# Kernel tuning notes

Measured on AMD Instinct MI355X. Metric: run time of the kernel, lower is better.

Reference implementation:

```python
import jax, jax.numpy as jnp
import numpy as np

# Semantic hierarchy configuration (stand-in for semantic_softmax_processor)
GROUP_SIZES = [8192, 4096, 2048, 1024, 512, 256, 128, 64, 32, 16]
NORM_FACTORS = [0.1] * len(GROUP_SIZES)
TOPK_CAP = 500
TEMPERATURE = 1.0
TOTAL_CLASSES = sum(GROUP_SIZES)  # 16368
BATCH = 1024


def setup_inputs() -> dict:
    key = jax.random.key(0)
    k1, k2, k3 = jax.random.split(key, 3)
    logits = jax.random.normal(k1, (BATCH, TOTAL_CLASSES), dtype=jnp.float32)
    logits_teacher = jax.random.normal(k2, (BATCH, TOTAL_CLASSES), dtype=jnp.float32)
    targets = jax.random.randint(k3, (BATCH,), 0, TOTAL_CLASSES, dtype=jnp.int64)
    return {"logits": logits, "logits_teacher": logits_teacher, "targets": targets}


def _group_kd_loss(s_logits, t_logits, temperature):
    # s_logits, t_logits: [B, C_i] for one semantic group
    B, C = t_logits.shape
    k = min(C, TOPK_CAP)
    # teacher top-k classes (sorted, largest)
    t_top, t_idx = jax.lax.top_k(t_logits, k)                 # [B, k]
    s_top = jnp.take_along_axis(s_logits, t_idx, axis=1)      # [B, k]
    log_p = jax.nn.log_softmax(s_top / temperature, axis=1)   # student log-probs
    log_q = jax.nn.log_softmax(t_top / temperature, axis=1)   # teacher log-probs
    q = jnp.exp(log_q)
    # KL(q || p), reduction='batchmean'
    kl = jnp.sum(q * (log_q - log_p)) / B
    return kl * temperature * temperature


def reference(logits, logits_teacher, targets):
    # targets are converted to semantic targets in the original module but are
    # never used in the loss computation (dead code) -> no effect on output.
    del targets
    total = jnp.float32(0.0)
    offset = 0
    for gsize, norm in zip(GROUP_SIZES, NORM_FACTORS):
        s_i = jax.lax.slice_in_dim(logits, offset, offset + gsize, axis=1)
        t_i = jax.lax.slice_in_dim(logits_teacher, offset, offset + gsize, axis=1)
        total = total + _group_kd_loss(s_i, t_i, TEMPERATURE) * norm
        offset += gsize
    return total
```

## Files before the change

### kernel.cpp

```cpp
#include <hip/hip_runtime.h>
#include <stdint.h>
#include <float.h>

#define TOTAL 16368
#define KSEL 500
#define Q0CAP 384
#define Q1CAP 704
#define G2CAP 768
#define NBUCKET 64

#define A_KV 0
#define A_SV 6144
#define A_IX 12288
#define B_KV 0
#define B_SV 5632
#define B_IX 11264
#define B_G2V 14080
#define B_G2I 17152
#define SMEM_BYTES 18688

__device__ __forceinline__ uint32_t fkey(float f) {
    uint32_t u = __float_as_uint(f);
    return (u & 0x80000000u) ? ~u : (u | 0x80000000u);
}
__device__ __forceinline__ float keyf(uint32_t k) {
    uint32_t u = (k & 0x80000000u) ? (k & 0x7FFFFFFFu) : ~k;
    return __uint_as_float(u);
}
__device__ __forceinline__ int lanerank(uint64_t m) {
    return __builtin_amdgcn_mbcnt_hi((uint32_t)(m >> 32),
           __builtin_amdgcn_mbcnt_lo((uint32_t)m, 0));
}
__device__ __forceinline__ int wave_sumi(int v) {
    #pragma unroll
    for (int o = 32; o > 0; o >>= 1) v += __shfl_xor(v, o, 64);
    return v;
}
__device__ __forceinline__ float wave_sumf(float v) {
    #pragma unroll
    for (int o = 32; o > 0; o >>= 1) v += __shfl_xor(v, o, 64);
    return v;
}
__device__ __forceinline__ float wave_maxf(float v) {
    #pragma unroll
    for (int o = 32; o > 0; o >>= 1) v = fmaxf(v, __shfl_xor(v, o, 64));
    return v;
}
__device__ __forceinline__ void lse_merge(float& m, float& l, float m2, float l2) {
    float M = fmaxf(m, m2);
    l = l * __expf(m - M) + l2 * __expf(m2 - M);
    m = M;
}

__device__ __noinline__ float wave_slow_kl(const float* __restrict__ t,
                                           const float* __restrict__ s, int C) {
    const int lane = threadIdx.x & 63;
    uint64_t lo = 0ull, hi = (1ull << 45), tau = 0ull;
    int cl = C, ch = 0;
    #pragma unroll 1
    for (int it = 0; it < 100; ++it) {
        uint64_t span = hi - lo;
        if (span <= 1ull) { tau = lo; break; }
        uint64_t mid;
        if (it & 1) mid = lo + (span >> 1);
        else {
            uint64_t st = span * (uint64_t)(cl - KSEL) / (uint64_t)(cl - ch);
            if (st < 1) st = 1;
            if (st > span - 1) st = span - 1;
            mid = lo + st;
        }
        int c = 0;
        #pragma unroll 1
        for (int i = lane; i < C; i += 64) {
            uint64_t ck = ((uint64_t)fkey(t[i]) << 13) | (uint64_t)(8191 - i);
            c += (ck > mid);
        }
        c = wave_sumi(c);
        if (c == KSEL) { tau = mid; break; }
        if (c > KSEL) { lo = mid; cl = c; } else { hi = mid; ch = c; }
    }
    float tmx = -FLT_MAX;
    for (int i = lane; i < C; i += 64) tmx = fmaxf(tmx, t[i]);
    tmx = wave_maxf(tmx);
    float St = 0.f, Stt = 0.f, Sts = 0.f, sm = -FLT_MAX;
    #pragma unroll 1
    for (int i = lane; i < C; i += 64) {
        float x = t[i];
        uint64_t ck = ((uint64_t)fkey(x) << 13) | (uint64_t)(8191 - i);
        if (ck > tau) {
            float e = __expf(x - tmx), v = s[i];
            St += e; Stt += e * x; Sts += e * v;
            sm = fmaxf(sm, v);
        }
    }
    St = wave_sumf(St); Stt = wave_sumf(Stt); Sts = wave_sumf(Sts); sm = wave_maxf(sm);
    float Ss = 0.f;
    #pragma unroll 1
    for (int i = lane; i < C; i += 64) {
        uint64_t ck = ((uint64_t)fkey(t[i]) << 13) | (uint64_t)(8191 - i);
        if (ck > tau) Ss += __expf(s[i] - sm);
    }
    Ss = wave_sumf(Ss);
    if (lane == 0)
        return (Stt - Sts) / St - tmx - __logf(St) + sm + __logf(Ss);
    return 0.f;
}

template <int CAP>
__device__ int slice_compact(const float* __restrict__ tq,
                             const float* __restrict__ sg,
                             float thr, int idx_off,
                             uint32_t* kv, float* sv, uint16_t* ix) {
    const int lane = threadIdx.x & 63;
    const float4* t4 = (const float4*)tq;
    float4 tb[8];
    #pragma unroll
    for (int u = 0; u < 8; ++u) tb[u] = t4[u * 64 + lane];
    int cnt = 0;
    #pragma unroll
    for (int u = 0; u < 8; ++u) {
        float tx[4] = {tb[u].x, tb[u].y, tb[u].z, tb[u].w};
        #pragma unroll
        for (int q = 0; q < 4; ++q) {
            bool p = tx[q] > thr;
            uint64_t m = __ballot(p);
            if (p) {
                int ofs = cnt + lanerank(m);
                if (ofs < CAP) {
                    kv[ofs] = fkey(tx[q]);
                    ix[ofs] = (uint16_t)((((u * 64 + lane) << 2) + q) + idx_off);
                }
            }
            cnt += (int)__popcll(m);
        }
    }
    if (cnt <= CAP) {
        for (int p = cnt + lane; p < CAP; p += 64) kv[p] = 0u;
        constexpr int NR = CAP / 64;
        float r[NR];
        #pragma unroll
        for (int j = 0; j < NR; ++j) {
            int p = lane + j * 64;
            r[j] = (p < cnt) ? sg[(int)ix[p]] : 0.f;
        }
        #pragma unroll
        for (int j = 0; j < NR; ++j) {
            int p = lane + j * 64;
            if (p < cnt) sv[p] = r[j];
        }
    }
    return cnt;
}

template <int S, int SEGCAP, int NS>
__device__ float seg_select(const uint32_t* __restrict__ kv,
                            const float* __restrict__ sv,
                            const uint16_t* __restrict__ ix,
                            const int* __restrict__ cnts, int C,
                            const float* __restrict__ tg,
                            const float* __restrict__ sg) {
    const int lane = threadIdx.x & 63;
    int tot = 0; bool bad = false;
    #pragma unroll
    for (int q = 0; q < S; ++q) {
        int c = cnts[q];
        tot += c;
        bad = bad || (c > SEGCAP);
    }
    if (bad || tot < KSEL) return wave_slow_kl(tg, sg, C);

    uint32_t key[NS];
    #pragma unroll
    for (int j = 0; j < NS; ++j) key[j] = kv[lane + j * 64];

    uint32_t kmx = 0u, kmn = 0xFFFFFFFFu;
    #pragma unroll
    for (int j = 0; j < NS; ++j) {
        uint32_t k = key[j];
        kmx = k > kmx ? k : kmx;
        if (k) kmn = k < kmn ? k : kmn;
    }
    #pragma unroll
    for (int o = 32; o > 0; o >>= 1) {
        uint32_t a = __shfl_xor(kmx, o, 64); kmx = a > kmx ? a : kmx;
        uint32_t b = __shfl_xor(kmn, o, 64); kmn = b < kmn ? b : kmn;
    }
    const float tmax = keyf(kmx);

    uint32_t lo = kmn - 1u, hi = kmx, tauhi = kmx;
    int cl = tot, ch = 0, cut = -1;
    bool exact = false;
    #pragma unroll 1
    for (int it = 0; it < 80; ++it) {
        uint32_t span = hi - lo;
        if (span <= 1u) break;
        uint32_t mid;
        if (!(it & 1)) {
            uint64_t st = (uint64_t)span * (uint32_t)(cl - KSEL) / (uint32_t)(cl - ch);
            if (st < 1) st = 1;
            if (st > span - 1) st = span - 1;
            mid = lo + (uint32_t)st;
        } else mid = lo + (span >> 1);
        int c = 0;
        #pragma unroll
        for (int j = 0; j < NS; ++j)
            c += (int)__popcll(__ballot(key[j] > mid));
        if (c == KSEL) { tauhi = mid; exact = true; break; }
        if (c > KSEL) { lo = mid; cl = c; } else { hi = mid; ch = c; }
    }
    if (!exact) {
        tauhi = hi;
        const int nT = KSEL - ch, nTie = cl - ch;
        if (nT >= nTie) cut = 0x7FFFFFFF;
        else {
            int l = -1, h = C - 1;
            #pragma unroll 1
            while (h - l > 1) {
                int m = (l + h) >> 1;
                int c = 0;
                #pragma unroll
                for (int j = 0; j < NS; ++j)
                    c += (int)__popcll(__ballot(key[j] == tauhi &&
                                                (int)ix[lane + j * 64] <= m));
                if (c >= nT) h = m; else l = m;
            }
            cut = h;
        }
    }

    uint32_t selm = 0u;
    if (cut == -1) {
        #pragma unroll
        for (int j = 0; j < NS; ++j) selm |= (key[j] > tauhi ? 1u : 0u) << j;
    } else if (cut == 0x7FFFFFFF) {
        #pragma unroll
        for (int j = 0; j < NS; ++j) selm |= (key[j] >= tauhi ? 1u : 0u) << j;
    } else {
        #pragma unroll
        for (int j = 0; j < NS; ++j) {
            bool sj = (key[j] > tauhi) ||
                      (key[j] == tauhi && (int)ix[lane + j * 64] <= cut);
            selm |= (sj ? 1u : 0u) << j;
        }
    }

    float St = 0.f, Stt = 0.f, Sts = 0.f, sm = -FLT_MAX;
    #pragma unroll
    for (int j = 0; j < NS; ++j) {
        if (selm & (1u << j)) {
            float tv = keyf(key[j]);
            float e = __expf(tv - tmax);
            float s = sv[lane + j * 64];
            St += e; Stt += e * tv; Sts += e * s;
            sm = fmaxf(sm, s);
        }
    }
    #pragma unroll
    for (int o = 32; o > 0; o >>= 1) {
        St  += __shfl_xor(St,  o, 64);
        Stt += __shfl_xor(Stt, o, 64);
        Sts += __shfl_xor(Sts, o, 64);
        sm = fmaxf(sm, __shfl_xor(sm, o, 64));
    }
    float Ss = 0.f;
    #pragma unroll
    for (int j = 0; j < NS; ++j)
        if (selm & (1u << j)) Ss += __expf(sv[lane + j * 64] - sm);
    Ss = wave_sumf(Ss);
    if (lane == 0)
        return (Stt - Sts) / St - tmax - __logf(St) + sm + __logf(Ss);
    return 0.f;
}

template <int NF4, int CAPT, int NST>
__device__ float big_wave(const float* __restrict__ tg, const float* __restrict__ s,
                          float thr, float* vals, uint16_t* idxs) {
    const int lane = threadIdx.x & 63;
    const float4* t4 = (const float4*)tg;
    constexpr int NB = NF4 / 8;
    int cnt = 0;
    float4 buf[8], nxt[8];
    #pragma unroll
    for (int u = 0; u < 8; ++u) buf[u] = t4[u * 64 + lane];
    #pragma unroll 1
    for (int b = 0; b < NB; ++b) {
        if (b + 1 < NB) {
            #pragma unroll
            for (int u = 0; u < 8; ++u)
                nxt[u] = t4[((b + 1) * 8 + u) * 64 + lane];
        }
        #pragma unroll
        for (int u = 0; u < 8; ++u) {
            float xs[4] = {buf[u].x, buf[u].y, buf[u].z, buf[u].w};
            #pragma unroll
            for (int q = 0; q < 4; ++q) {
                bool p = xs[q] > thr;
                uint64_t m = __ballot(p);
                if (p) {
                    int ofs = cnt + lanerank(m);
                    if (ofs < CAPT) {
                        vals[ofs] = xs[q];
                        idxs[ofs] = (uint16_t)((((b * 8 + u) * 64 + lane) << 2) + q);
                    }
                }
                cnt += (int)__popcll(m);
            }
        }
        if (b + 1 < NB) {
            #pragma unroll
            for (int u = 0; u < 8; ++u) buf[u] = nxt[u];
        }
    }
    if (cnt < KSEL || cnt > CAPT) return wave_slow_kl(tg, s, NF4 * 256);

    uint32_t key[NST];
    #pragma unroll
    for (int j = 0; j < NST; ++j) {
        int p = lane + j * 64;
        key[j] = (p < cnt) ? fkey(vals[p]) : 0u;
    }
    uint32_t kmx = 0u, kmn = 0xFFFFFFFFu;
    #pragma unroll
    for (int j = 0; j < NST; ++j) {
        uint32_t k = key[j];
        kmx = k > kmx ? k : kmx;
        if (k) kmn = k < kmn ? k : kmn;
    }
    #pragma unroll
    for (int o = 32; o > 0; o >>= 1) {
        uint32_t a = __shfl_xor(kmx, o, 64); kmx = a > kmx ? a : kmx;
        uint32_t b2 = __shfl_xor(kmn, o, 64); kmn = b2 < kmn ? b2 : kmn;
    }
    const float tmax = keyf(kmx);

    uint32_t lo = kmn - 1u, hi = kmx, tauhi = kmx;
    int cl = cnt, ch = 0, cut = -1;
    bool exact = false;
    #pragma unroll 1
    for (int it = 0; it < 80; ++it) {
        uint32_t span = hi - lo;
        if (span <= 1u) break;
        uint32_t mid;
        if (!(it & 1)) {
            uint64_t st = (uint64_t)span * (uint32_t)(cl - KSEL) / (uint32_t)(cl - ch);
            if (st < 1) st = 1;
            if (st > span - 1) st = span - 1;
            mid = lo + (uint32_t)st;
        } else mid = lo + (span >> 1);
        int c = 0;
        #pragma unroll
        for (int j = 0; j < NST; ++j)
            c += (int)__popcll(__ballot(key[j] > mid));
        if (c == KSEL) { tauhi = mid; exact = true; break; }
        if (c > KSEL) { lo = mid; cl = c; } else { hi = mid; ch = c; }
    }
    if (!exact) {
        tauhi = hi;
        const int nT = KSEL - ch, nTie = cl - ch;
        if (nT >= nTie) cut = 0x7FFFFFFF;
        else {
            int idxr[NST];
            #pragma unroll
            for (int j = 0; j < NST; ++j) {
                int p = lane + j * 64;
                idxr[j] = (p < cnt) ? (int)idxs[p] : 0x7FFF;
            }
            int l = -1, h = 8191;
            #pragma unroll 1
            while (h - l > 1) {
                int m = (l + h) >> 1;
                int c = 0;
                #pragma unroll
                for (int j = 0; j < NST; ++j)
                    c += (int)__popcll(__ballot(key[j] == tauhi && idxr[j] <= m));
                if (c >= nT) h = m; else l = m;
            }
            cut = h;
        }
    }

    uint32_t selm = 0u;
    if (cut == -1) {
        #pragma unroll
        for (int j = 0; j < NST; ++j) selm |= (key[j] > tauhi ? 1u : 0u) << j;
    } else if (cut == 0x7FFFFFFF) {
        #pragma unroll
        for (int j = 0; j < NST; ++j) selm |= (key[j] >= tauhi ? 1u : 0u) << j;
    } else {
        #pragma unroll
        for (int j = 0; j < NST; ++j) {
            int p = lane + j * 64;
            bool sj = (key[j] > tauhi) ||
                      (key[j] == tauhi && p < cnt && (int)idxs[p] <= cut);
            selm |= (sj ? 1u : 0u) << j;
        }
    }

    float svc[NST];
    #pragma unroll
    for (int j = 0; j < NST; ++j)
        svc[j] = (selm & (1u << j)) ? s[(int)idxs[lane + j * 64]] : 0.f;

    float St = 0.f, Stt = 0.f, Sts = 0.f, sm = -FLT_MAX;
    #pragma unroll
    for (int j = 0; j < NST; ++j) {
        if (selm & (1u << j)) {
            float tv = keyf(key[j]);
            float e = __expf(tv - tmax);
            St += e; Stt += e * tv; Sts += e * svc[j];
            sm = fmaxf(sm, svc[j]);
        }
    }
    #pragma unroll
    for (int o = 32; o > 0; o >>= 1) {
        St  += __shfl_xor(St,  o, 64);
        Stt += __shfl_xor(Stt, o, 64);
        Sts += __shfl_xor(Sts, o, 64);
        sm = fmaxf(sm, __shfl_xor(sm, o, 64));
    }
    float Ss = 0.f;
    #pragma unroll
    for (int j = 0; j < NST; ++j)
        if (selm & (1u << j)) Ss += __expf(svc[j] - sm);
    Ss = wave_sumf(Ss);
    if (lane == 0)
        return (Stt - Sts) / St - tmax - __logf(St) + sm + __logf(Ss);
    return 0.f;
}

template <int NS, class IdxF>
__device__ float select_accum(uint32_t (&key)[NS], IdxF idxOf, const float* svp) {
    const int lane = threadIdx.x & 63;
    uint32_t kmx = 0u, kmn = 0xFFFFFFFFu;
    #pragma unroll
    for (int j = 0; j < NS; ++j) {
        uint32_t k = key[j];
        kmx = k > kmx ? k : kmx;
        kmn = k < kmn ? k : kmn;
    }
    #pragma unroll
    for (int o = 32; o > 0; o >>= 1) {
        uint32_t a = __shfl_xor(kmx, o, 64); kmx = a > kmx ? a : kmx;
        uint32_t b = __shfl_xor(kmn, o, 64); kmn = b < kmn ? b : kmn;
    }
    const float tmax = keyf(kmx);

    uint32_t lo = kmn - 1u, hi = kmx, tauhi = kmx;
    int cl = NS * 64, ch = 0, cut = -1;
    bool exact = false;
    #pragma unroll 1
    for (int it = 0; it < 80; ++it) {
        uint32_t span = hi - lo;
        if (span <= 1u) break;
        uint32_t mid;
        if (!(it & 1)) {
            uint64_t st = (uint64_t)span * (uint32_t)(cl - KSEL) / (uint32_t)(cl - ch);
            if (st < 1) st = 1;
            if (st > span - 1) st = span - 1;
            mid = lo + (uint32_t)st;
        } else mid = lo + (span >> 1);
        int c = 0;
        #pragma unroll
        for (int j = 0; j < NS; ++j)
            c += (int)__popcll(__ballot(key[j] > mid));
        if (c == KSEL) { tauhi = mid; exact = true; break; }
        if (c > KSEL) { lo = mid; cl = c; } else { hi = mid; ch = c; }
    }
    if (!exact) {
        tauhi = hi;
        const int nT = KSEL - ch, nTie = cl - ch;
        if (nT >= nTie) cut = 0x7FFFFFFF;
        else {
            int l = -1, h = NS * 64 - 1;
            #pragma unroll 1
            while (h - l > 1) {
                int m = (l + h) >> 1;
                int c = 0;
                #pragma unroll
                for (int j = 0; j < NS; ++j)
                    c += (int)__popcll(__ballot(key[j] == tauhi && idxOf(j) <= m));
                if (c >= nT) h = m; else l = m;
            }
            cut = h;
        }
    }

    float St = 0.f, Stt = 0.f, Sts = 0.f, sm = -FLT_MAX;
    #pragma unroll
    for (int j = 0; j < NS; ++j) {
        uint32_t kj = key[j];
        bool sj = (kj > tauhi) || (kj == tauhi && idxOf(j) <= cut);
        if (sj) {
            float tv = keyf(kj);
            float e = __expf(tv - tmax);
            St += e; Stt += e * tv; Sts += e * svp[j];
            sm = fmaxf(sm, svp[j]);
        }
    }
    #pragma unroll
    for (int o = 32; o > 0; o >>= 1) {
        St  += __shfl_xor(St,  o, 64);
        Stt += __shfl_xor(Stt, o, 64);
        Sts += __shfl_xor(Sts, o, 64);
        sm = fmaxf(sm, __shfl_xor(sm, o, 64));
    }
    float Ss = 0.f;
    #pragma unroll
    for (int j = 0; j < NS; ++j) {
        uint32_t kj = key[j];
        bool sj = (kj > tauhi) || (kj == tauhi && idxOf(j) <= cut);
        if (sj) Ss += __expf(svp[j] - sm);
    }
    Ss = wave_sumf(Ss);
    if (lane == 0)
        return (Stt - Sts) / St - tmax - __logf(St) + sm + __logf(Ss);
    return 0.f;
}

template <int NJ>
__device__ float mid_wave(const float* __restrict__ t, const float* __restrict__ s) {
    const int lane = threadIdx.x & 63;
    const float4* t4 = (const float4*)t;
    const float4* s4 = (const float4*)s;
    uint32_t key[NJ];
    float svp[NJ];
    #pragma unroll
    for (int c = 0; c < NJ / 4; ++c) {
        float4 x = t4[lane + c * 64];
        float4 y = s4[lane + c * 64];
        key[4 * c + 0] = fkey(x.x); key[4 * c + 1] = fkey(x.y);
        key[4 * c + 2] = fkey(x.z); key[4 * c + 3] = fkey(x.w);
        svp[4 * c + 0] = y.x; svp[4 * c + 1] = y.y;
        svp[4 * c + 2] = y.z; svp[4 * c + 3] = y.w;
    }
    auto idxOf = [&](int j) { return ((lane + (j >> 2) * 64) << 2) + (j & 3); };
    return select_accum<NJ>(key, idxOf, svp);
}

__device__ float tiny_group(const float* __restrict__ t, const float* __restrict__ s,
                            int Cg) {
    const int lane = threadIdx.x & 63;
    float St = 0.f, Stt = 0.f, Sts = 0.f, m = -FLT_MAX, l = 0.f;
    float tv[4], svv[4];
    #pragma unroll
    for (int q = 0; q < 4; ++q) {
        int i = lane + q * 64;
        bool va = i < Cg;
        tv[q] = va ? t[i] : -FLT_MAX;
        svv[q] = va ? s[i] : 0.f;
    }
    float mx = -FLT_MAX;
    #pragma unroll
    for (int q = 0; q < 4; ++q) mx = fmaxf(mx, tv[q]);
    mx = wave_maxf(mx);
    #pragma unroll
    for (int q = 0; q < 4; ++q) {
        if (lane + q * 64 < Cg) {
            float e = __expf(tv[q] - mx);
            St += e; Stt += e * tv[q]; Sts += e * svv[q];
            float x = svv[q];
            if (x > m) { l = l * __expf(m - x) + 1.f; m = x; }
            else       { l += __expf(x - m); }
        }
    }
    #pragma unroll
    for (int o = 32; o > 0; o >>= 1) {
        St  += __shfl_xor(St,  o, 64);
        Stt += __shfl_xor(Stt, o, 64);
        Sts += __shfl_xor(Sts, o, 64);
        float m2 = __shfl_xor(m, o, 64);
        float l2 = __shfl_xor(l, o, 64);
        lse_merge(m, l, m2, l2);
    }
    if (lane == 0)
        return (Stt - Sts) / St - mx - __logf(St) + m + __logf(l);
    return 0.f;
}

__global__ __launch_bounds__(256, 6) void kd_coop(const float* __restrict__ sL,
                                                  const float* __restrict__ tL,
                                                  float* __restrict__ partial) {
    __shared__ char smem[SMEM_BYTES] __attribute__((aligned(16)));
    __shared__ int cnts[4];
    const int bid = blockIdx.x;
    const int w = threadIdx.x >> 6;
    const int lane = threadIdx.x & 63;
    const bool typeA = bid < 1024;
    const int row = typeA ? bid : bid - 1024;
    const float* tr = tL + (size_t)row * TOTAL;
    const float* sr = sL + (size_t)row * TOTAL;

    float kl = 0.f;

    if (typeA) {
        uint32_t* kv = (uint32_t*)(smem + A_KV);
        float*    sv = (float*)(smem + A_SV);
        uint16_t* ix = (uint16_t*)(smem + A_IX);
        int c = slice_compact<Q0CAP>(tr + w * 2048, sr, 1.10f, w * 2048,
                                     kv + w * Q0CAP, sv + w * Q0CAP, ix + w * Q0CAP);
        if (lane == 0) cnts[w] = c;
    } else {
        if (w < 2) {
            uint32_t* kv = (uint32_t*)(smem + B_KV);
            float*    sv = (float*)(smem + B_SV);
            uint16_t* ix = (uint16_t*)(smem + B_IX);
            int c = slice_compact<Q1CAP>(tr + 8192 + w * 2048, sr + 8192, 0.60f,
                                         w * 2048,
                                         kv + w * Q1CAP, sv + w * Q1CAP,
                                         ix + w * Q1CAP);
            if (lane == 0) cnts[w] = c;
        } else if (w == 2) {
            float*    g2v = (float*)(smem + B_G2V);
            uint16_t* g2i = (uint16_t*)(smem + B_G2I);
            kl = big_wave<8, G2CAP, 12>(tr + 12288, sr + 12288, 0.50f, g2v, g2i);
        } else {
            kl  = mid_wave<16>(tr + 14336, sr + 14336);
            kl += mid_wave<8>(tr + 15360, sr + 15360);
            kl += tiny_group(tr + 15872, sr + 15872, 256);
            kl += tiny_group(tr + 16128, sr + 16128, 128);
            kl += tiny_group(tr + 16256, sr + 16256, 64);
            kl += tiny_group(tr + 16320, sr + 16320, 32);
            kl += tiny_group(tr + 16352, sr + 16352, 16);
        }
    }

    __syncthreads();

    if (w == 0) {
        if (typeA)
            kl += seg_select<4, Q0CAP, 24>((uint32_t*)(smem + A_KV),
                                           (float*)(smem + A_SV),
                                           (uint16_t*)(smem + A_IX),
                                           cnts, 8192, tr, sr);
        else
            kl += seg_select<2, Q1CAP, 22>((uint32_t*)(smem + B_KV),
                                           (float*)(smem + B_SV),
                                           (uint16_t*)(smem + B_IX),
                                           cnts, 4096, tr + 8192, sr + 8192);
    }

    if (lane == 0)
        atomicAdd(&partial[(row + w * 16 + (typeA ? 0 : 8)) & (NBUCKET - 1)],
                  kl * (0.1f / 1024.f));
}

__global__ void zero_ws(float* partial) {
    if (threadIdx.x < NBUCKET) partial[threadIdx.x] = 0.f;
}

__global__ void final_sum(const float* __restrict__ partial, float* __restrict__ out) {
    float v = (threadIdx.x < NBUCKET) ? partial[threadIdx.x] : 0.f;
    #pragma unroll
    for (int o = 32; o > 0; o >>= 1) v += __shfl_down(v, o, 64);
    if (threadIdx.x == 0) out[0] = v;
}

extern "C" void kernel_launch(void* const* d_in, const int* in_sizes, int n_in,
                              void* d_out, int out_size, void* d_ws, size_t ws_size,
                              hipStream_t stream) {
    (void)in_sizes; (void)n_in; (void)ws_size; (void)out_size;
    const float* s = (const float*)d_in[0];
    const float* t = (const float*)d_in[1];
    float* out = (float*)d_out;
    float* ws = (float*)d_ws;

    hipLaunchKernelGGL(zero_ws, dim3(1), dim3(64), 0, stream, ws);
    hipLaunchKernelGGL(kd_coop, dim3(2048), dim3(256), 0, stream, s, t, ws);
    hipLaunchKernelGGL(final_sum, dim3(1), dim3(64), 0, stream, ws, out);
}
```

Measured before the change: 184.5 us.

## Repartition row work into three 2-wave block types with lazy student gathers

Replaces the two 4-wave block types with three 2-wave block types per row. Group 0 is now compacted by two waves of 4096 elements each, with double-buffered loads. Group 1 moves to a single-wave big_wave path, and the mid and tiny groups get their own block. Student values are gathered only for the selected top-k entries after selection, instead of for every compacted candidate. The goal is to balance per-wave work and cut shared-memory writes and gather traffic, at the cost of more blocks and a longer serial path per wave.

After: 177.6 us. -3.7%, faster.

```diff
diff --git a/kernel.cpp b/kernel.cpp
--- a/kernel.cpp
+++ b/kernel.cpp
@@ -4,20 +4,9 @@
 
 #define TOTAL 16368
 #define KSEL 500
-#define Q0CAP 384
-#define Q1CAP 704
-#define G2CAP 768
+#define HQ 704
+#define NSH 22
 #define NBUCKET 64
-
-#define A_KV 0
-#define A_SV 6144
-#define A_IX 12288
-#define B_KV 0
-#define B_SV 5632
-#define B_IX 11264
-#define B_G2V 14080
-#define B_G2I 17152
-#define SMEM_BYTES 18688
 
 __device__ __forceinline__ uint32_t fkey(float f) {
     uint32_t u = __float_as_uint(f);
@@ -103,172 +92,6 @@
     Ss = wave_sumf(Ss);
     if (lane == 0)
         return (Stt - Sts) / St - tmx - __logf(St) + sm + __logf(Ss);
-    return 0.f;
-}
-
-template <int CAP>
-__device__ int slice_compact(const float* __restrict__ tq,
-                             const float* __restrict__ sg,
-                             float thr, int idx_off,
-                             uint32_t* kv, float* sv, uint16_t* ix) {
-    const int lane = threadIdx.x & 63;
-    const float4* t4 = (const float4*)tq;
-    float4 tb[8];
-    #pragma unroll
-    for (int u = 0; u < 8; ++u) tb[u] = t4[u * 64 + lane];
-    int cnt = 0;
-    #pragma unroll
-    for (int u = 0; u < 8; ++u) {
-        float tx[4] = {tb[u].x, tb[u].y, tb[u].z, tb[u].w};
-        #pragma unroll
-        for (int q = 0; q < 4; ++q) {
-            bool p = tx[q] > thr;
-            uint64_t m = __ballot(p);
-            if (p) {
-                int ofs = cnt + lanerank(m);
-                if (ofs < CAP) {
-                    kv[ofs] = fkey(tx[q]);
-                    ix[ofs] = (uint16_t)((((u * 64 + lane) << 2) + q) + idx_off);
-                }
-            }
-            cnt += (int)__popcll(m);
-        }
-    }
-    if (cnt <= CAP) {
-        for (int p = cnt + lane; p < CAP; p += 64) kv[p] = 0u;
-        constexpr int NR = CAP / 64;
-        float r[NR];
-        #pragma unroll
-        for (int j = 0; j < NR; ++j) {
-            int p = lane + j * 64;
-            r[j] = (p < cnt) ? sg[(int)ix[p]] : 0.f;
-        }
-        #pragma unroll
-        for (int j = 0; j < NR; ++j) {
-            int p = lane + j * 64;
-            if (p < cnt) sv[p] = r[j];
-        }
-    }
-    return cnt;
-}
-
-template <int S, int SEGCAP, int NS>
-__device__ float seg_select(const uint32_t* __restrict__ kv,
-                            const float* __restrict__ sv,
-                            const uint16_t* __restrict__ ix,
-                            const int* __restrict__ cnts, int C,
-                            const float* __restrict__ tg,
-                            const float* __restrict__ sg) {
-    const int lane = threadIdx.x & 63;
-    int tot = 0; bool bad = false;
-    #pragma unroll
-    for (int q = 0; q < S; ++q) {
-        int c = cnts[q];
-        tot += c;
-        bad = bad || (c > SEGCAP);
-    }
-    if (bad || tot < KSEL) return wave_slow_kl(tg, sg, C);
-
-    uint32_t key[NS];
-    #pragma unroll
-    for (int j = 0; j < NS; ++j) key[j] = kv[lane + j * 64];
-
-    uint32_t kmx = 0u, kmn = 0xFFFFFFFFu;
-    #pragma unroll
-    for (int j = 0; j < NS; ++j) {
-        uint32_t k = key[j];
-        kmx = k > kmx ? k : kmx;
-        if (k) kmn = k < kmn ? k : kmn;
-    }
-    #pragma unroll
-    for (int o = 32; o > 0; o >>= 1) {
-        uint32_t a = __shfl_xor(kmx, o, 64); kmx = a > kmx ? a : kmx;
-        uint32_t b = __shfl_xor(kmn, o, 64); kmn = b < kmn ? b : kmn;
-    }
-    const float tmax = keyf(kmx);
-
-    uint32_t lo = kmn - 1u, hi = kmx, tauhi = kmx;
-    int cl = tot, ch = 0, cut = -1;
-    bool exact = false;
-    #pragma unroll 1
-    for (int it = 0; it < 80; ++it) {
-        uint32_t span = hi - lo;
-        if (span <= 1u) break;
-        uint32_t mid;
-        if (!(it & 1)) {
-            uint64_t st = (uint64_t)span * (uint32_t)(cl - KSEL) / (uint32_t)(cl - ch);
-            if (st < 1) st = 1;
-            if (st > span - 1) st = span - 1;
-            mid = lo + (uint32_t)st;
-        } else mid = lo + (span >> 1);
-        int c = 0;
-        #pragma unroll
-        for (int j = 0; j < NS; ++j)
-            c += (int)__popcll(__ballot(key[j] > mid));
-        if (c == KSEL) { tauhi = mid; exact = true; break; }
-        if (c > KSEL) { lo = mid; cl = c; } else { hi = mid; ch = c; }
-    }
-    if (!exact) {
-        tauhi = hi;
-        const int nT = KSEL - ch, nTie = cl - ch;
-        if (nT >= nTie) cut = 0x7FFFFFFF;
-        else {
-            int l = -1, h = C - 1;
-            #pragma unroll 1
-            while (h - l > 1) {
-                int m = (l + h) >> 1;
-                int c = 0;
-                #pragma unroll
-                for (int j = 0; j < NS; ++j)
-                    c += (int)__popcll(__ballot(key[j] == tauhi &&
-                                                (int)ix[lane + j * 64] <= m));
-                if (c >= nT) h = m; else l = m;
-            }
-            cut = h;
-        }
-    }
-
-    uint32_t selm = 0u;
-    if (cut == -1) {
-        #pragma unroll
-        for (int j = 0; j < NS; ++j) selm |= (key[j] > tauhi ? 1u : 0u) << j;
-    } else if (cut == 0x7FFFFFFF) {
-        #pragma unroll
-        for (int j = 0; j < NS; ++j) selm |= (key[j] >= tauhi ? 1u : 0u) << j;
-    } else {
-        #pragma unroll
-        for (int j = 0; j < NS; ++j) {
-            bool sj = (key[j] > tauhi) ||
-                      (key[j] == tauhi && (int)ix[lane + j * 64] <= cut);
-            selm |= (sj ? 1u : 0u) << j;
-        }
-    }
-
-    float St = 0.f, Stt = 0.f, Sts = 0.f, sm = -FLT_MAX;
-    #pragma unroll
-    for (int j = 0; j < NS; ++j) {
-        if (selm & (1u << j)) {
-            float tv = keyf(key[j]);
-            float e = __expf(tv - tmax);
-            float s = sv[lane + j * 64];
-            St += e; Stt += e * tv; Sts += e * s;
-            sm = fmaxf(sm, s);
-        }
-    }
-    #pragma unroll
-    for (int o = 32; o > 0; o >>= 1) {
-        St  += __shfl_xor(St,  o, 64);
-        Stt += __shfl_xor(Stt, o, 64);
-        Sts += __shfl_xor(Sts, o, 64);
-        sm = fmaxf(sm, __shfl_xor(sm, o, 64));
-    }
-    float Ss = 0.f;
-    #pragma unroll
-    for (int j = 0; j < NS; ++j)
-        if (selm & (1u << j)) Ss += __expf(sv[lane + j * 64] - sm);
-    Ss = wave_sumf(Ss);
-    if (lane == 0)
-        return (Stt - Sts) / St - tmax - __logf(St) + sm + __logf(Ss);
     return 0.f;
 }
 
@@ -428,6 +251,165 @@
     return 0.f;
 }
 
+__device__ int half_compact(const float* __restrict__ tq, int idx_off,
+                            uint32_t* kv, uint16_t* ix) {
+    const int lane = threadIdx.x & 63;
+    const float4* t4 = (const float4*)tq;
+    int cnt = 0;
+    float4 buf[8], nxt[8];
+    #pragma unroll
+    for (int u = 0; u < 8; ++u) buf[u] = t4[u * 64 + lane];
+    #pragma unroll 1
+    for (int b = 0; b < 2; ++b) {
+        if (b == 0) {
+            #pragma unroll
+            for (int u = 0; u < 8; ++u) nxt[u] = t4[(8 + u) * 64 + lane];
+        }
+        #pragma unroll
+        for (int u = 0; u < 8; ++u) {
+            float xs[4] = {buf[u].x, buf[u].y, buf[u].z, buf[u].w};
+            #pragma unroll
+            for (int q = 0; q < 4; ++q) {
+                bool p = xs[q] > 1.10f;
+                uint64_t m = __ballot(p);
+                if (p) {
+                    int ofs = cnt + lanerank(m);
+                    if (ofs < HQ) {
+                        kv[ofs] = fkey(xs[q]);
+                        ix[ofs] = (uint16_t)(((((b * 8 + u) * 64 + lane) << 2) + q)
+                                             + idx_off);
+                    }
+                }
+                cnt += (int)__popcll(m);
+            }
+        }
+        if (b == 0) {
+            #pragma unroll
+            for (int u = 0; u < 8; ++u) buf[u] = nxt[u];
+        }
+    }
+    if (cnt <= HQ)
+        for (int p = cnt + lane; p < HQ; p += 64) kv[p] = 0u;
+    return cnt;
+}
+
+__device__ float pair_select(const uint32_t* __restrict__ kv,
+                             const uint16_t* __restrict__ ix,
+                             const int* __restrict__ cnts,
+                             const float* __restrict__ tg,
+                             const float* __restrict__ sg) {
+    const int lane = threadIdx.x & 63;
+    const int tot = cnts[0] + cnts[1];
+    if (cnts[0] > HQ || cnts[1] > HQ || tot < KSEL)
+        return wave_slow_kl(tg, sg, 8192);
+
+    uint32_t key[NSH];
+    #pragma unroll
+    for (int j = 0; j < NSH; ++j) key[j] = kv[lane + j * 64];
+
+    uint32_t kmx = 0u, kmn = 0xFFFFFFFFu;
+    #pragma unroll
+    for (int j = 0; j < NSH; ++j) {
+        uint32_t k = key[j];
+        kmx = k > kmx ? k : kmx;
+        if (k) kmn = k < kmn ? k : kmn;
+    }
+    #pragma unroll
+    for (int o = 32; o > 0; o >>= 1) {
+        uint32_t a = __shfl_xor(kmx, o, 64); kmx = a > kmx ? a : kmx;
+        uint32_t b2 = __shfl_xor(kmn, o, 64); kmn = b2 < kmn ? b2 : kmn;
+    }
+    const float tmax = keyf(kmx);
+
+    uint32_t lo = kmn - 1u, hi = kmx, tauhi = kmx;
+    int cl = tot, ch = 0, cut = -1;
+    bool exact = false;
+    #pragma unroll 1
+    for (int it = 0; it < 80; ++it) {
+        uint32_t span = hi - lo;
+        if (span <= 1u) break;
+        uint32_t mid;
+        if (!(it & 1)) {
+            uint64_t st = (uint64_t)span * (uint32_t)(cl - KSEL) / (uint32_t)(cl - ch);
+            if (st < 1) st = 1;
+            if (st > span - 1) st = span - 1;
+            mid = lo + (uint32_t)st;
+        } else mid = lo + (span >> 1);
+        int c = 0;
+        #pragma unroll
+        for (int j = 0; j < NSH; ++j)
+            c += (int)__popcll(__ballot(key[j] > mid));
+        if (c == KSEL) { tauhi = mid; exact = true; break; }
+        if (c > KSEL) { lo = mid; cl = c; } else { hi = mid; ch = c; }
+    }
+    if (!exact) {
+        tauhi = hi;
+        const int nT = KSEL - ch, nTie = cl - ch;
+        if (nT >= nTie) cut = 0x7FFFFFFF;
+        else {
+            int l = -1, h = 8191;
+            #pragma unroll 1
+            while (h - l > 1) {
+                int m = (l + h) >> 1;
+                int c = 0;
+                #pragma unroll
+                for (int j = 0; j < NSH; ++j)
+                    c += (int)__popcll(__ballot(key[j] == tauhi &&
+                                                (int)ix[lane + j * 64] <= m));
+                if (c >= nT) h = m; else l = m;
+            }
+            cut = h;
+        }
+    }
+
+    uint32_t selm = 0u;
+    if (cut == -1) {
+        #pragma unroll
+        for (int j = 0; j < NSH; ++j) selm |= (key[j] > tauhi ? 1u : 0u) << j;
+    } else if (cut == 0x7FFFFFFF) {
+        #pragma unroll
+        for (int j = 0; j < NSH; ++j) selm |= (key[j] >= tauhi ? 1u : 0u) << j;
+    } else {
+        #pragma unroll
+        for (int j = 0; j < NSH; ++j) {
+            bool sj = (key[j] > tauhi) ||
+                      (key[j] == tauhi && (int)ix[lane + j * 64] <= cut);
+            selm |= (sj ? 1u : 0u) << j;
+        }
+    }
+
+    float svc[NSH];
+    #pragma unroll
+    for (int j = 0; j < NSH; ++j)
+        svc[j] = (selm & (1u << j)) ? sg[(int)ix[lane + j * 64]] : 0.f;
+
+    float St = 0.f, Stt = 0.f, Sts = 0.f, sm = -FLT_MAX;
+    #pragma unroll
+    for (int j = 0; j < NSH; ++j) {
+        if (selm & (1u << j)) {
+            float tv = keyf(key[j]);
+            float e = __expf(tv - tmax);
+            St += e; Stt += e * tv; Sts += e * svc[j];
+            sm = fmaxf(sm, svc[j]);
+        }
+    }
+    #pragma unroll
+    for (int o = 32; o > 0; o >>= 1) {
+        St  += __shfl_xor(St,  o, 64);
+        Stt += __shfl_xor(Stt, o, 64);
+        Sts += __shfl_xor(Sts, o, 64);
+        sm = fmaxf(sm, __shfl_xor(sm, o, 64));
+    }
+    float Ss = 0.f;
+    #pragma unroll
+    for (int j = 0; j < NSH; ++j)
+        if (selm & (1u << j)) Ss += __expf(svc[j] - sm);
+    Ss = wave_sumf(Ss);
+    if (lane == 0)
+        return (Stt - Sts) / St - tmax - __logf(St) + sm + __logf(Ss);
+    return 0.f;
+}
+
 template <int NS, class IdxF>
 __device__ float select_accum(uint32_t (&key)[NS], IdxF idxOf, const float* svp) {
     const int lane = threadIdx.x & 63;
@@ -577,45 +559,44 @@
     return 0.f;
 }
 
-__global__ __launch_bounds__(256, 6) void kd_coop(const float* __restrict__ sL,
-                                                  const float* __restrict__ tL,
-                                                  float* __restrict__ partial) {
-    __shared__ char smem[SMEM_BYTES] __attribute__((aligned(16)));
-    __shared__ int cnts[4];
+__global__ __launch_bounds__(128, 6) void kd_mix(const float* __restrict__ sL,
+                                                 const float* __restrict__ tL,
+                                                 float* __restrict__ partial) {
+    __shared__ char smem[12544] __attribute__((aligned(16)));
+    __shared__ int cnts[2];
     const int bid = blockIdx.x;
     const int w = threadIdx.x >> 6;
     const int lane = threadIdx.x & 63;
-    const bool typeA = bid < 1024;
-    const int row = typeA ? bid : bid - 1024;
+    const int type = bid >> 10;
+    const int row = bid & 1023;
     const float* tr = tL + (size_t)row * TOTAL;
     const float* sr = sL + (size_t)row * TOTAL;
 
     float kl = 0.f;
 
-    if (typeA) {
-        uint32_t* kv = (uint32_t*)(smem + A_KV);
-        float*    sv = (float*)(smem + A_SV);
-        uint16_t* ix = (uint16_t*)(smem + A_IX);
-        int c = slice_compact<Q0CAP>(tr + w * 2048, sr, 1.10f, w * 2048,
-                                     kv + w * Q0CAP, sv + w * Q0CAP, ix + w * Q0CAP);
+    if (type == 0) {
+        uint32_t* kv = (uint32_t*)smem;
+        uint16_t* ix = (uint16_t*)(smem + 5632);
+        int c = half_compact(tr + w * 4096, w * 4096, kv + w * HQ, ix + w * HQ);
         if (lane == 0) cnts[w] = c;
+        __syncthreads();
+        if (w == 0)
+            kl = pair_select(kv, ix, cnts, tr, sr);
+    } else if (type == 1) {
+        if (w == 0) {
+            float*    v1 = (float*)smem;
+            uint16_t* i1 = (uint16_t*)(smem + 5120);
+            kl = big_wave<16, 1280, 20>(tr + 8192, sr + 8192, 0.60f, v1, i1);
+        } else {
+            float*    v2 = (float*)(smem + 7680);
+            uint16_t* i2 = (uint16_t*)(smem + 10752);
+            kl = big_wave<8, 768, 12>(tr + 12288, sr + 12288, 0.50f, v2, i2);
+        }
     } else {
-        if (w < 2) {
-            uint32_t* kv = (uint32_t*)(smem + B_KV);
-            float*    sv = (float*)(smem + B_SV);
-            uint16_t* ix = (uint16_t*)(smem + B_IX);
-            int c = slice_compact<Q1CAP>(tr + 8192 + w * 2048, sr + 8192, 0.60f,
-                                         w * 2048,
-                                         kv + w * Q1CAP, sv + w * Q1CAP,
-                                         ix + w * Q1CAP);
-            if (lane == 0) cnts[w] = c;
-        } else if (w == 2) {
-            float*    g2v = (float*)(smem + B_G2V);
-            uint16_t* g2i = (uint16_t*)(smem + B_G2I);
-            kl = big_wave<8, G2CAP, 12>(tr + 12288, sr + 12288, 0.50f, g2v, g2i);
+        if (w == 0) {
+            kl = mid_wave<16>(tr + 14336, sr + 14336);
         } else {
-            kl  = mid_wave<16>(tr + 14336, sr + 14336);
-            kl += mid_wave<8>(tr + 15360, sr + 15360);
+            kl  = mid_wave<8>(tr + 15360, sr + 15360);
             kl += tiny_group(tr + 15872, sr + 15872, 256);
             kl += tiny_group(tr + 16128, sr + 16128, 128);
             kl += tiny_group(tr + 16256, sr + 16256, 64);
@@ -624,23 +605,8 @@
         }
     }
 
-    __syncthreads();
-
-    if (w == 0) {
-        if (typeA)
-            kl += seg_select<4, Q0CAP, 24>((uint32_t*)(smem + A_KV),
-                                           (float*)(smem + A_SV),
-                                           (uint16_t*)(smem + A_IX),
-                                           cnts, 8192, tr, sr);
-        else
-            kl += seg_select<2, Q1CAP, 22>((uint32_t*)(smem + B_KV),
-                                           (float*)(smem + B_SV),
-                                           (uint16_t*)(smem + B_IX),
-                                           cnts, 4096, tr + 8192, sr + 8192);
-    }
-
     if (lane == 0)
-        atomicAdd(&partial[(row + w * 16 + (typeA ? 0 : 8)) & (NBUCKET - 1)],
+        atomicAdd(&partial[(row + type * 21 + w * 37) & (NBUCKET - 1)],
                   kl * (0.1f / 1024.f));
 }
 
@@ -665,6 +631,6 @@
     float* ws = (float*)d_ws;
 
     hipLaunchKernelGGL(zero_ws, dim3(1), dim3(64), 0, stream, ws);
-    hipLaunchKernelGGL(kd_coop, dim3(2048), dim3(256), 0, stream, s, t, ws);
+    hipLaunchKernelGGL(kd_mix, dim3(3072), dim3(128), 0, stream, s, t, ws);
     hipLaunchKernelGGL(final_sum, dim3(1), dim3(64), 0, stream, ws, out);
 }
```
